# Kernel optimization log

Hardware: AMD Instinct MI355X
Metric: run time of the kernel (lower is better)

The kernel has to match this reference:

```python
import jax, jax.numpy as jnp
import numpy as np

NUM_ATLAS = 100000
FD = 16
FS = 9  # fsize + 1
NV, NB = 65536, 8


def setup_inputs() -> dict:
    key = jax.random.key(0)
    k1, k2, k3 = jax.random.split(key, 3)
    x = jax.random.uniform(k1, (NV, NB, 2), minval=-1.0, maxval=1.0, dtype=jnp.float32)
    inds = jax.random.randint(k2, (NV, NB), 0, NUM_ATLAS)
    ft = jax.random.normal(k3, (NUM_ATLAS, FD, FS, FS), dtype=jnp.float32) * 0.1
    return {"x": x, "inds": inds, "ft": ft}


def reference(x, inds, ft):
    # Fused equivalent of: ft[inds] -> (Nv*Nb, fd, fs, fs) then
    # F.grid_sample(..., align_corners=True, padding_mode='border') at one point.
    # We index the 4 bilinear corners directly in the atlas (no big gather).
    fs = ft.shape[-1]
    # grid coords: x[...,0] -> width (last axis), x[...,1] -> height
    # align_corners=True: pix = (c + 1) / 2 * (fs - 1); border padding == clamp
    gx = jnp.clip((x[..., 0] + 1.0) * 0.5 * (fs - 1), 0.0, fs - 1.0)
    gy = jnp.clip((x[..., 1] + 1.0) * 0.5 * (fs - 1), 0.0, fs - 1.0)
    x0f = jnp.floor(gx)
    y0f = jnp.floor(gy)
    wx = (gx - x0f)[..., None]  # (Nv, Nb, 1)
    wy = (gy - y0f)[..., None]
    x0 = x0f.astype(jnp.int32)
    y0 = y0f.astype(jnp.int32)
    x1 = jnp.minimum(x0 + 1, fs - 1)
    y1 = jnp.minimum(y0 + 1, fs - 1)
    # advanced indexing with a slice in the middle -> (Nv, Nb, fd)
    v00 = ft[inds, :, y0, x0]
    v01 = ft[inds, :, y0, x1]
    v10 = ft[inds, :, y1, x0]
    v11 = ft[inds, :, y1, x1]
    top = v00 * (1.0 - wx) + v01 * wx
    bot = v10 * (1.0 - wx) + v11 * wx
    return top * (1.0 - wy) + bot * wy  # (Nv, Nb, fd)
```

## Files before the change

kernel.cpp:

```cpp
#include <hip/hip_runtime.h>


constexpr int FD = 16;
constexpr int FS = 9;
constexpr int NSAMP = 65536 * 8;
constexpr int NUM_ATLAS = 100000;
constexpr int BLOCK = 256;

constexpr int SCAN_CHUNK = 1024;
constexpr int NUM_SCAN_BLOCKS = (NUM_ATLAS + SCAN_CHUNK - 1) / SCAN_CHUNK;
constexpr int PARTIALS_PAD = 128;

__global__ __launch_bounds__(BLOCK) void hist_kernel(const int* __restrict__ inds,
                                                     int* __restrict__ hist) {
    int i = blockIdx.x * BLOCK + threadIdx.x;
    if (i < NSAMP) atomicAdd(&hist[inds[i]], 1);
}

__global__ __launch_bounds__(BLOCK) void scanA_kernel(const int* __restrict__ hist,
                                                      int* __restrict__ offsets,
                                                      int* __restrict__ partials) {
    __shared__ int lds[BLOCK];
    int t = threadIdx.x;
    int base = blockIdx.x * SCAN_CHUNK + t * 4;
    int v[4];
    #pragma unroll
    for (int j = 0; j < 4; ++j) v[j] = (base + j < NUM_ATLAS) ? hist[base + j] : 0;
    int sum = v[0] + v[1] + v[2] + v[3];
    lds[t] = sum;
    __syncthreads();
    for (int off = 1; off < BLOCK; off <<= 1) {
        int add = (t >= off) ? lds[t - off] : 0;
        __syncthreads();
        lds[t] += add;
        __syncthreads();
    }
    int incl = lds[t];
    int excl = incl - sum;
    if (t == BLOCK - 1) partials[blockIdx.x] = incl;
    int run = excl;
    #pragma unroll
    for (int j = 0; j < 4; ++j) {
        if (base + j < NUM_ATLAS) offsets[base + j] = run;
        run += v[j];
    }
}

__global__ void scanB_kernel(int* __restrict__ partials) {
    if (threadIdx.x == 0) {
        int run = 0;
        for (int i = 0; i < NUM_SCAN_BLOCKS; ++i) {
            int v = partials[i];
            partials[i] = run;
            run += v;
        }
    }
}

__global__ __launch_bounds__(BLOCK) void scanC_kernel(int* __restrict__ offsets,
                                                      const int* __restrict__ partials) {
    int i = blockIdx.x * BLOCK + threadIdx.x;
    if (i < NUM_ATLAS) offsets[i] += partials[i / SCAN_CHUNK];
}

__global__ __launch_bounds__(BLOCK) void scatter_kernel(const int* __restrict__ inds,
                                                        int* __restrict__ offsets,
                                                        int* __restrict__ order) {
    int i = blockIdx.x * BLOCK + threadIdx.x;
    if (i < NSAMP) {
        int ind = inds[i];
        int pos = atomicAdd(&offsets[ind], 1);
        order[pos] = i;
    }
}

__global__ __launch_bounds__(BLOCK) void gather_kernel(
    const float2* __restrict__ x,
    const int*    __restrict__ inds,
    const float*  __restrict__ ft,
    const int*    __restrict__ order,
    float4*       __restrict__ out)
{
    int tid = blockIdx.x * BLOCK + threadIdx.x;
    int s = order[tid >> 2];
    int c0 = (tid & 3) * 4;

    float2 xy = x[s];
    int ind   = inds[s];

    const float fsm1 = (float)(FS - 1);
    float gx = fminf(fmaxf((xy.x + 1.0f) * 0.5f * fsm1, 0.0f), fsm1);
    float gy = fminf(fmaxf((xy.y + 1.0f) * 0.5f * fsm1, 0.0f), fsm1);

    int x0 = (int)floorf(gx);
    int y0 = (int)floorf(gy);
    x0 = min(x0, FS - 2);
    y0 = min(y0, FS - 2);
    float wx = gx - (float)x0;
    float wy = gy - (float)y0;

    float w00 = (1.0f - wx) * (1.0f - wy);
    float w01 = wx * (1.0f - wy);
    float w10 = (1.0f - wx) * wy;
    float w11 = wx * wy;

    const float* base = ft + (size_t)ind * (FD * FS * FS)
                           + (size_t)c0 * (FS * FS)
                           + y0 * FS + x0;

    float r[4];
    #pragma unroll
    for (int i = 0; i < 4; ++i) {
        const float* p = base + i * (FS * FS);
        float v00 = p[0];
        float v01 = p[1];
        float v10 = p[FS];
        float v11 = p[FS + 1];
        r[i] = v00 * w00 + v01 * w01 + v10 * w10 + v11 * w11;
    }

    out[(size_t)s * 4 + (tid & 3)] = make_float4(r[0], r[1], r[2], r[3]);
}

extern "C" void kernel_launch(void* const* d_in, const int* in_sizes, int n_in,
                              void* d_out, int out_size, void* d_ws, size_t ws_size,
                              hipStream_t stream) {
    const float2* x    = (const float2*)d_in[0];
    const int*    inds = (const int*)d_in[1];
    const float*  ft   = (const float*)d_in[2];
    float4*       out  = (float4*)d_out;

    int* ws       = (int*)d_ws;
    int* hist     = ws;
    int* partials = hist + NUM_ATLAS;
    int* offsets  = partials + PARTIALS_PAD;
    int* order    = offsets + NUM_ATLAS;

    hipMemsetAsync(hist, 0, (size_t)(NUM_ATLAS + PARTIALS_PAD) * sizeof(int), stream);

    hist_kernel<<<(NSAMP + BLOCK - 1) / BLOCK, BLOCK, 0, stream>>>(inds, hist);
    scanA_kernel<<<NUM_SCAN_BLOCKS, BLOCK, 0, stream>>>(hist, offsets, partials);
    scanB_kernel<<<1, 64, 0, stream>>>(partials);
    scanC_kernel<<<(NUM_ATLAS + BLOCK - 1) / BLOCK, BLOCK, 0, stream>>>(offsets, partials);
    scatter_kernel<<<(NSAMP + BLOCK - 1) / BLOCK, BLOCK, 0, stream>>>(inds, offsets, order);

    int gather_threads = NSAMP * 4;
    gather_kernel<<<gather_threads / BLOCK, BLOCK, 0, stream>>>(x, inds, ft, order, out);
}
```

Baseline: 736.8 us.

## Gather per atlas entry: stage entry in LDS, process its samples per wave

Restructures the gather so each wavefront owns one atlas entry. The wave copies the whole 16x9x9 entry into LDS once, then interpolates every sample that maps to that entry from LDS, using the scatter-advanced offsets as segment ends. This replaces four scattered global corner loads per channel per sample with one coalesced entry load. It also parallelises the single-thread partial scan with an LDS scan. The catch is that it loads every entry that has at least one sample, and uneven segment sizes leave waves idle.

```diff
diff --git a/kernel.cpp b/kernel.cpp
--- a/kernel.cpp
+++ b/kernel.cpp
@@ -3,13 +3,17 @@
 
 constexpr int FD = 16;
 constexpr int FS = 9;
+constexpr int ENTRY_FLOATS = FD * FS * FS;
+constexpr int ENTRY_F4     = ENTRY_FLOATS / 4;
 constexpr int NSAMP = 65536 * 8;
 constexpr int NUM_ATLAS = 100000;
 constexpr int BLOCK = 256;
+constexpr int WAVES_PER_BLOCK = 4;
 
 constexpr int SCAN_CHUNK = 1024;
 constexpr int NUM_SCAN_BLOCKS = (NUM_ATLAS + SCAN_CHUNK - 1) / SCAN_CHUNK;
 constexpr int PARTIALS_PAD = 128;
+
 
 __global__ __launch_bounds__(BLOCK) void hist_kernel(const int* __restrict__ inds,
                                                      int* __restrict__ hist) {
@@ -46,15 +50,19 @@
     }
 }
 
-__global__ void scanB_kernel(int* __restrict__ partials) {
-    if (threadIdx.x == 0) {
-        int run = 0;
-        for (int i = 0; i < NUM_SCAN_BLOCKS; ++i) {
-            int v = partials[i];
-            partials[i] = run;
-            run += v;
-        }
+__global__ __launch_bounds__(128) void scanB_kernel(int* __restrict__ partials) {
+    __shared__ int lds[128];
+    int t = threadIdx.x;
+    int v = (t < NUM_SCAN_BLOCKS) ? partials[t] : 0;
+    lds[t] = v;
+    __syncthreads();
+    for (int off = 1; off < 128; off <<= 1) {
+        int add = (t >= off) ? lds[t - off] : 0;
+        __syncthreads();
+        lds[t] += add;
+        __syncthreads();
     }
+    if (t < NUM_SCAN_BLOCKS) partials[t] = lds[t] - v;
 }
 
 __global__ __launch_bounds__(BLOCK) void scanC_kernel(int* __restrict__ offsets,
@@ -76,50 +84,59 @@
 
 __global__ __launch_bounds__(BLOCK) void gather_kernel(
     const float2* __restrict__ x,
-    const int*    __restrict__ inds,
     const float*  __restrict__ ft,
     const int*    __restrict__ order,
-    float4*       __restrict__ out)
+    const int*    __restrict__ hist,
+    const int*    __restrict__ seg_end,
+    float*        __restrict__ out)
 {
-    int tid = blockIdx.x * BLOCK + threadIdx.x;
-    int s = order[tid >> 2];
-    int c0 = (tid & 3) * 4;
+    __shared__ float4 tile[WAVES_PER_BLOCK][ENTRY_F4];
+    const int wv   = threadIdx.x >> 6;
+    const int lane = threadIdx.x & 63;
+    const int e    = blockIdx.x * WAVES_PER_BLOCK + wv;
 
-    float2 xy = x[s];
-    int ind   = inds[s];
+    const int end   = seg_end[e];
+    const int cnt   = hist[e];
+    const int start = end - cnt;
 
+    if (cnt > 0) {
+        const float4* src = (const float4*)(ft + (size_t)e * ENTRY_FLOATS);
+        #pragma unroll
+        for (int k = 0; k < 5; ++k)
+            tile[wv][lane + 64 * k] = src[lane + 64 * k];
+        if (lane < ENTRY_F4 - 320)
+            tile[wv][320 + lane] = src[320 + lane];
+    }
+    __syncthreads();
+
+    if (cnt == 0) return;
+
+    const float* L  = (const float*)tile[wv];
+    const int ch    = lane & 15;
+    const int sub   = lane >> 4;
     const float fsm1 = (float)(FS - 1);
-    float gx = fminf(fmaxf((xy.x + 1.0f) * 0.5f * fsm1, 0.0f), fsm1);
-    float gy = fminf(fmaxf((xy.y + 1.0f) * 0.5f * fsm1, 0.0f), fsm1);
 
-    int x0 = (int)floorf(gx);
-    int y0 = (int)floorf(gy);
-    x0 = min(x0, FS - 2);
-    y0 = min(y0, FS - 2);
-    float wx = gx - (float)x0;
-    float wy = gy - (float)y0;
+    for (int p = start + sub; p < end; p += 4) {
+        int sid = order[p];
+        float2 xy = x[sid];
 
-    float w00 = (1.0f - wx) * (1.0f - wy);
-    float w01 = wx * (1.0f - wy);
-    float w10 = (1.0f - wx) * wy;
-    float w11 = wx * wy;
+        float gx = fminf(fmaxf((xy.x + 1.0f) * 0.5f * fsm1, 0.0f), fsm1);
+        float gy = fminf(fmaxf((xy.y + 1.0f) * 0.5f * fsm1, 0.0f), fsm1);
+        int x0 = min((int)gx, FS - 2);
+        int y0 = min((int)gy, FS - 2);
+        float wx = gx - (float)x0;
+        float wy = gy - (float)y0;
+        float w00 = (1.0f - wx) * (1.0f - wy);
+        float w01 = wx * (1.0f - wy);
+        float w10 = (1.0f - wx) * wy;
+        float w11 = wx * wy;
 
-    const float* base = ft + (size_t)ind * (FD * FS * FS)
-                           + (size_t)c0 * (FS * FS)
-                           + y0 * FS + x0;
+        int base = ch * (FS * FS) + y0 * FS + x0;
+        float r = L[base]          * w00 + L[base + 1]      * w01
+                + L[base + FS]     * w10 + L[base + FS + 1] * w11;
 
-    float r[4];
-    #pragma unroll
-    for (int i = 0; i < 4; ++i) {
-        const float* p = base + i * (FS * FS);
-        float v00 = p[0];
-        float v01 = p[1];
-        float v10 = p[FS];
-        float v11 = p[FS + 1];
-        r[i] = v00 * w00 + v01 * w01 + v10 * w10 + v11 * w11;
+        out[(size_t)sid * FD + ch] = r;
     }
-
-    out[(size_t)s * 4 + (tid & 3)] = make_float4(r[0], r[1], r[2], r[3]);
 }
 
 extern "C" void kernel_launch(void* const* d_in, const int* in_sizes, int n_in,
@@ -128,7 +145,7 @@
     const float2* x    = (const float2*)d_in[0];
     const int*    inds = (const int*)d_in[1];
     const float*  ft   = (const float*)d_in[2];
-    float4*       out  = (float4*)d_out;
+    float*        out  = (float*)d_out;
 
     int* ws       = (int*)d_ws;
     int* hist     = ws;
@@ -136,14 +153,14 @@
     int* offsets  = partials + PARTIALS_PAD;
     int* order    = offsets + NUM_ATLAS;
 
-    hipMemsetAsync(hist, 0, (size_t)(NUM_ATLAS + PARTIALS_PAD) * sizeof(int), stream);
+    hipMemsetAsync(hist, 0, (size_t)NUM_ATLAS * sizeof(int), stream);
 
-    hist_kernel<<<(NSAMP + BLOCK - 1) / BLOCK, BLOCK, 0, stream>>>(inds, hist);
+    hist_kernel<<<NSAMP / BLOCK, BLOCK, 0, stream>>>(inds, hist);
     scanA_kernel<<<NUM_SCAN_BLOCKS, BLOCK, 0, stream>>>(hist, offsets, partials);
-    scanB_kernel<<<1, 64, 0, stream>>>(partials);
+    scanB_kernel<<<1, 128, 0, stream>>>(partials);
     scanC_kernel<<<(NUM_ATLAS + BLOCK - 1) / BLOCK, BLOCK, 0, stream>>>(offsets, partials);
-    scatter_kernel<<<(NSAMP + BLOCK - 1) / BLOCK, BLOCK, 0, stream>>>(inds, offsets, order);
+    scatter_kernel<<<NSAMP / BLOCK, BLOCK, 0, stream>>>(inds, offsets, order);
 
-    int gather_threads = NSAMP * 4;
-    gather_kernel<<<gather_threads / BLOCK, BLOCK, 0, stream>>>(x, inds, ft, order, out);
+    gather_kernel<<<NUM_ATLAS / WAVES_PER_BLOCK, BLOCK, 0, stream>>>(
+        x, ft, order, hist, offsets, out);
 }
```

Measured after the change: 735.5 us. No clear change (-0.2%).
